# Kernel tuning notes

Measured on AMD Instinct MI355X. Metric: run time of the kernel, lower is better.

Reference implementation:

```python
import jax, jax.numpy as jnp
import numpy as np

N = 100000
E = 600000
H = 128
G = 64          # number of graphs
LN_EPS = 1e-5


def setup_inputs() -> dict:
    key = jax.random.key(0)
    ks = jax.random.split(key, 16)
    node = jax.random.normal(ks[0], (N, H), dtype=jnp.float32)
    edge_index = jax.random.randint(ks[1], (2, E), 0, N, dtype=jnp.int64)
    edge_attr = jax.random.normal(ks[2], (E, 1), dtype=jnp.float32)
    batch_ptr = jnp.sort(jax.random.randint(ks[3], (N,), 0, G, dtype=jnp.int64))
    s = 1.0 / np.sqrt(H)
    params = dict(
        eps=jnp.float32(0.0),  # GINConv train_eps=True, init 0
        W1=jax.random.uniform(ks[4], (H, H), jnp.float32, -s, s),
        b1=jnp.zeros((H,), jnp.float32),
        g1=jnp.ones((H,), jnp.float32), be1=jnp.zeros((H,), jnp.float32),
        W2=jax.random.uniform(ks[5], (H, H), jnp.float32, -s, s),
        b2=jnp.zeros((H,), jnp.float32),
        g2=jnp.ones((H,), jnp.float32), be2=jnp.zeros((H,), jnp.float32),
        W3=jax.random.uniform(ks[6], (H, H), jnp.float32, -s, s),
        b3=jnp.zeros((H,), jnp.float32),
        ln_w=jnp.ones((H,), jnp.float32), ln_b=jnp.zeros((H,), jnp.float32),
    )
    return dict(node=node, edge_index=edge_index, edge_attr=edge_attr,
                batch_ptr=batch_ptr, **params)


def _layernorm(x, g, b):
    mu = x.mean(-1, keepdims=True)
    var = ((x - mu) ** 2).mean(-1, keepdims=True)
    return (x - mu) * jax.lax.rsqrt(var + LN_EPS) * g + b


def _forward(node, edge_index, batch_ptr, eps, W1, b1, g1, be1, W2, b2, g2, be2,
             W3, b3, ln_w, ln_b):
    src, dst = edge_index[0], edge_index[1]
    # GIN sum aggregation: scatter-add neighbor features to targets
    agg = jax.ops.segment_sum(node[src], dst, num_segments=N)  # [N, H]
    h = (1.0 + eps) * node + agg
    # 3-layer MLP (PyG MLP: lin -> LayerNorm -> ReLU, final lin plain)
    h = jax.nn.relu(_layernorm(h @ W1 + b1, g1, be1))
    h = jax.nn.relu(_layernorm(h @ W2 + b2, g2, be2))
    h = h @ W3 + b3
    # PyG graph-mode LayerNorm: normalize over all nodes+features per graph
    cnt = jax.ops.segment_sum(jnp.ones((N,), h.dtype), batch_ptr, num_segments=G)
    norm = jnp.maximum(cnt * H, 1.0)                       # [G]
    mean = jax.ops.segment_sum(h.sum(-1), batch_ptr, num_segments=G) / norm
    hc = h - mean[batch_ptr][:, None]
    var = jax.ops.segment_sum((hc * hc).sum(-1), batch_ptr, num_segments=G) / norm
    out = hc * jax.lax.rsqrt(var + LN_EPS)[batch_ptr][:, None] * ln_w + ln_b
    return jax.nn.relu(out)


def reference(node, edge_index, edge_attr, batch_ptr, eps, W1, b1, g1, be1,
              W2, b2, g2, be2, W3, b3, ln_w, ln_b):
    del edge_attr  # accepted by GIN_Layer.forward but unused
    return _forward(node, edge_index, batch_ptr, eps, W1, b1, g1, be1,
                    W2, b2, g2, be2, W3, b3, ln_w, ln_b)
```

## Files before the change

kernel.cpp:

```cpp
#include <hip/hip_runtime.h>

#define N_NODES 100000
#define N_EDGES 600000
#define H 128
#define G_NUM 64
#define LN_EPS 1e-5f

#define WSTR 136

#define NTILES ((N_NODES + 63) / 64)

#define SCAN_CHUNK 1024
#define SCAN_NB ((N_NODES + SCAN_CHUNK - 1) / SCAN_CHUNK)
#define FILL_NB ((N_EDGES + 255) / 256)
#define WT_NB ((3 * 16384 + 255) / 256)
#define CONV_NB ((N_NODES * 64 + 255) / 256)

typedef __attribute__((ext_vector_type(8))) short short8;
typedef __attribute__((ext_vector_type(4))) float floatx4;

__device__ __forceinline__ unsigned short f2bf(float x) {
    unsigned int u = __float_as_uint(x);
    u += 0x7fffu + ((u >> 16) & 1u);
    return (unsigned short)(u >> 16);
}

__global__ __launch_bounds__(256) void hist_kernel(
    const int* __restrict__ ei, int* __restrict__ deg)
{
    int e = blockIdx.x * 256 + threadIdx.x;
    if (e >= N_EDGES) return;
    atomicAdd(&deg[ei[N_EDGES + e]], 1);
}

__global__ __launch_bounds__(256) void scan1_kernel(
    const int* __restrict__ deg, int* __restrict__ off,
    int* __restrict__ blksum)
{
    __shared__ int sA[256], sB[256];
    const int tid = threadIdx.x;
    const int base = blockIdx.x * SCAN_CHUNK + tid * 4;
    int v[4];
#pragma unroll
    for (int j = 0; j < 4; ++j) {
        int i = base + j;
        v[j] = (i < N_NODES) ? deg[i] : 0;
    }
    int tsum = v[0] + v[1] + v[2] + v[3];
    int* a = sA; int* b = sB;
    a[tid] = tsum;
    __syncthreads();
#pragma unroll
    for (int o = 1; o < 256; o <<= 1) {
        int t = a[tid] + ((tid >= o) ? a[tid - o] : 0);
        b[tid] = t;
        __syncthreads();
        int* tmp = a; a = b; b = tmp;
    }
    int run = a[tid] - tsum;
#pragma unroll
    for (int j = 0; j < 4; ++j) {
        int i = base + j;
        if (i < N_NODES) off[i] = run;
        run += v[j];
    }
    if (tid == 255) blksum[blockIdx.x] = a[255];
}

__global__ __launch_bounds__(256) void scan23_kernel(
    int* __restrict__ off, const int* __restrict__ blksum,
    int* __restrict__ cursor)
{
    __shared__ int sA[128], sB[128];
    const int tid = threadIdx.x;
    if (tid < 128) sA[tid] = (tid < SCAN_NB) ? blksum[tid] : 0;
    __syncthreads();
    int* a = sA; int* b = sB;
#pragma unroll
    for (int o = 1; o < 128; o <<= 1) {
        int t = 0;
        if (tid < 128) t = a[tid] + ((tid >= o) ? a[tid - o] : 0);
        __syncthreads();
        if (tid < 128) b[tid] = t;
        __syncthreads();
        int* tmp = a; a = b; b = tmp;
    }
    int excl = 0;
    if (tid < 128) excl = a[tid] - ((tid < SCAN_NB) ? blksum[tid] : 0);
    __syncthreads();
    if (tid < 128) sA[tid] = excl;
    __syncthreads();

    int i = blockIdx.x * 256 + tid;
    if (i < N_NODES) {
        int val = off[i] + sA[i >> 10];
        off[i] = val;
        cursor[i] = val;
    }
    if (i == 0) off[N_NODES] = N_EDGES;
}

__global__ __launch_bounds__(256) void fill_wt_kernel(
    const int* __restrict__ ei, int* __restrict__ cursor,
    int* __restrict__ csr,
    const float* __restrict__ W1, const float* __restrict__ W2,
    const float* __restrict__ W3, unsigned short* __restrict__ WT,
    const float* __restrict__ node, unsigned int* __restrict__ nodeb)
{
    int gb = blockIdx.x;
    if (gb < FILL_NB) {
        int e = gb * 256 + threadIdx.x;
        if (e >= N_EDGES) return;
        int dst = ei[N_EDGES + e];
        int pos = atomicAdd(&cursor[dst], 1);
        csr[pos] = ei[e];
    } else if (gb < FILL_NB + WT_NB) {
        int idx = (gb - FILL_NB) * 256 + threadIdx.x;
        if (idx >= 3 * 16384) return;
        int l = idx >> 14, r = idx & 16383;
        int frag = r >> 3, j = r & 7;
        int lane = frag & 63, ktnt = frag >> 6;
        int kt = ktnt & 3, nt = ktnt >> 2;
        int c = lane & 15, q = lane >> 4;
        int n = nt * 16 + c;
        int k = kt * 32 + q * 8 + j;
        const float* W = (l == 0) ? W1 : ((l == 1) ? W2 : W3);
        WT[l * 16384 + r] = f2bf(W[k * 128 + n]);
    } else {
        int i = (gb - FILL_NB - WT_NB) * 256 + threadIdx.x;
        if (i >= N_NODES * 64) return;
        float2 v = ((const float2*)node)[i];
        nodeb[i] = (unsigned)f2bf(v.x) | ((unsigned)f2bf(v.y) << 16);
    }
}

__global__ __launch_bounds__(256, 8) void gather_kernel(
    const float* __restrict__ node, const unsigned int* __restrict__ nodeb,
    const int* __restrict__ off, const int* __restrict__ csr,
    const float* __restrict__ epsp, unsigned int* __restrict__ h0)
{
    const int wv = (blockIdx.x * 256 + threadIdx.x) >> 6;
    const int lane = threadIdx.x & 63;
    const int s0 = off[wv], s1 = off[wv + 1];
    const float epsv = 1.0f + epsp[0];
    float2 own = ((const float2*)node)[(size_t)wv * 64 + lane];
    float ax = epsv * own.x, ay = epsv * own.y;
    const int d = s1 - s0;

    for (int base = 0; base < d; base += 64) {
        int m = d - base; if (m > 64) m = 64;
        int idx = 0;
        if (lane < m) idx = csr[s0 + base + lane];
        int j = 0;
        if (nodeb) {
            for (; j + 4 <= m; j += 4) {
                int i0 = __shfl(idx, j),     i1 = __shfl(idx, j + 1);
                int i2 = __shfl(idx, j + 2), i3 = __shfl(idx, j + 3);
                unsigned v0 = nodeb[(size_t)i0 * 64 + lane];
                unsigned v1 = nodeb[(size_t)i1 * 64 + lane];
                unsigned v2 = nodeb[(size_t)i2 * 64 + lane];
                unsigned v3 = nodeb[(size_t)i3 * 64 + lane];
                ax += __uint_as_float(v0 << 16) + __uint_as_float(v1 << 16) +
                      __uint_as_float(v2 << 16) + __uint_as_float(v3 << 16);
                ay += __uint_as_float(v0 & 0xffff0000u) +
                      __uint_as_float(v1 & 0xffff0000u) +
                      __uint_as_float(v2 & 0xffff0000u) +
                      __uint_as_float(v3 & 0xffff0000u);
            }
            for (; j < m; ++j) {
                int i0 = __shfl(idx, j);
                unsigned v0 = nodeb[(size_t)i0 * 64 + lane];
                ax += __uint_as_float(v0 << 16);
                ay += __uint_as_float(v0 & 0xffff0000u);
            }
        } else {
            const float2* np2 = (const float2*)node;
            for (; j + 4 <= m; j += 4) {
                int i0 = __shfl(idx, j),     i1 = __shfl(idx, j + 1);
                int i2 = __shfl(idx, j + 2), i3 = __shfl(idx, j + 3);
                float2 v0 = np2[(size_t)i0 * 64 + lane];
                float2 v1 = np2[(size_t)i1 * 64 + lane];
                float2 v2 = np2[(size_t)i2 * 64 + lane];
                float2 v3 = np2[(size_t)i3 * 64 + lane];
                ax += v0.x + v1.x + v2.x + v3.x;
                ay += v0.y + v1.y + v2.y + v3.y;
            }
            for (; j < m; ++j) {
                int i0 = __shfl(idx, j);
                float2 v0 = np2[(size_t)i0 * 64 + lane];
                ax += v0.x; ay += v0.y;
            }
        }
    }
    h0[(size_t)wv * 64 + lane] = (unsigned)f2bf(ax) | ((unsigned)f2bf(ay) << 16);
}

__device__ __forceinline__ void gemm_frags(const unsigned short* __restrict__ hIn,
                                           const unsigned short* __restrict__ WTl,
                                           floatx4 acc[8], int w, int lane)
{
    const int c = lane & 15, q = lane >> 4;
#pragma unroll
    for (int nt = 0; nt < 8; ++nt) acc[nt] = (floatx4){0.f, 0.f, 0.f, 0.f};
#pragma unroll
    for (int kt = 0; kt < 4; ++kt) {
        short8 a = *(const short8*)&hIn[(w * 16 + c) * WSTR + kt * 32 + q * 8];
#pragma unroll
        for (int nt = 0; nt < 8; ++nt) {
            short8 b = *(const short8*)&WTl[(nt * 256 + kt * 64 + lane) * 8];
            acc[nt] = __builtin_amdgcn_mfma_f32_16x16x32_bf16(a, b, acc[nt], 0, 0, 0);
        }
    }
}

__device__ __forceinline__ void gemm_layer_ln(const unsigned short* __restrict__ hIn,
                                              unsigned short* __restrict__ hOut,
                                              const unsigned short* __restrict__ WTl,
                                              const float* __restrict__ bias,
                                              const float* __restrict__ g,
                                              const float* __restrict__ be,
                                              int w, int lane)
{
    const int c = lane & 15, q = lane >> 4;
    floatx4 acc[8];
    gemm_frags(hIn, WTl, acc, w, lane);

    float sum[4] = {0.f, 0.f, 0.f, 0.f};
    float sq[4]  = {0.f, 0.f, 0.f, 0.f};
#pragma unroll
    for (int nt = 0; nt < 8; ++nt) {
        float bv = bias[nt * 16 + c];
#pragma unroll
        for (int i = 0; i < 4; ++i) {
            float vv = acc[nt][i] + bv;
            acc[nt][i] = vv;
            sum[i] += vv; sq[i] += vv * vv;
        }
    }
#pragma unroll
    for (int m = 1; m < 16; m <<= 1) {
#pragma unroll
        for (int i = 0; i < 4; ++i) {
            sum[i] += __shfl_xor(sum[i], m);
            sq[i]  += __shfl_xor(sq[i], m);
        }
    }
    float mu[4], rstd[4];
#pragma unroll
    for (int i = 0; i < 4; ++i) {
        mu[i]   = sum[i] * (1.0f / 128.0f);
        rstd[i] = rsqrtf(sq[i] * (1.0f / 128.0f) - mu[i] * mu[i] + LN_EPS);
    }
#pragma unroll
    for (int nt = 0; nt < 8; ++nt) {
        float gw = g[nt * 16 + c];
        float bw = be[nt * 16 + c];
#pragma unroll
        for (int i = 0; i < 4; ++i) {
            float val = fmaxf(0.f, (acc[nt][i] - mu[i]) * rstd[i] * gw + bw);
            hOut[(w * 16 + q * 4 + i) * WSTR + nt * 16 + c] = f2bf(val);
        }
    }
}

__global__ __launch_bounds__(256, 4) void mlp_kernel(
    const unsigned int* __restrict__ h0, const unsigned short* __restrict__ WT,
    const float* __restrict__ b1, const float* __restrict__ g1,
    const float* __restrict__ be1,
    const float* __restrict__ b2, const float* __restrict__ g2,
    const float* __restrict__ be2,
    const float* __restrict__ b3, const int* __restrict__ batch,
    float* __restrict__ out, float* __restrict__ gstat)
{
    __shared__ unsigned short hA[64 * WSTR];
    __shared__ unsigned short hB[64 * WSTR];
    __shared__ float prm[7 * 128];
    __shared__ float s_gsum[G_NUM], s_gsq[G_NUM], s_gcnt[G_NUM];

    const int tid = threadIdx.x;
    const int w = tid >> 6, lane = tid & 63;
    const int row0 = blockIdx.x * 64;

    if (tid < G_NUM) { s_gsum[tid] = 0.f; s_gsq[tid] = 0.f; s_gcnt[tid] = 0.f; }
    {
        const float* srcs[7] = {b1, g1, be1, b2, g2, be2, b3};
#pragma unroll
        for (int t = 0; t < 4; ++t) {
            int i = tid + t * 256;
            if (i < 7 * 128) prm[i] = srcs[i >> 7][i & 127];
        }
    }

    {
        const int n0 = row0 + w * 16;
#pragma unroll
        for (int i = 0; i < 16; ++i) {
            int n = n0 + i;
            unsigned int pack = (n < N_NODES) ? h0[(size_t)n * 64 + lane] : 0u;
            ((unsigned int*)&hA[(w * 16 + i) * WSTR])[lane] = pack;
        }
    }
    __syncthreads();

    gemm_layer_ln(hA, hB, WT,         &prm[0],   &prm[128], &prm[256], w, lane);
    gemm_layer_ln(hB, hA, WT + 16384, &prm[384], &prm[512], &prm[640], w, lane);

    {
        const int c = lane & 15, q = lane >> 4;
        floatx4 acc3[8];
        gemm_frags(hA, WT + 32768, acc3, w, lane);
        float sum[4] = {0.f, 0.f, 0.f, 0.f};
        float sq[4]  = {0.f, 0.f, 0.f, 0.f};
#pragma unroll
        for (int nt = 0; nt < 8; ++nt) {
            float bv = prm[768 + nt * 16 + c];
#pragma unroll
            for (int i = 0; i < 4; ++i) {
                float vv = acc3[nt][i] + bv;
                size_t nrow = (size_t)row0 + w * 16 + q * 4 + i;
                if (nrow < N_NODES)
                    out[nrow * H + nt * 16 + c] = vv;
                sum[i] += vv; sq[i] += vv * vv;
            }
        }
#pragma unroll
        for (int m = 1; m < 16; m <<= 1) {
#pragma unroll
            for (int i = 0; i < 4; ++i) {
                sum[i] += __shfl_xor(sum[i], m);
                sq[i]  += __shfl_xor(sq[i], m);
            }
        }
        if (c == 0) {
#pragma unroll
            for (int i = 0; i < 4; ++i) {
                size_t nrow = (size_t)row0 + w * 16 + q * 4 + i;
                if (nrow < N_NODES) {
                    int g = batch[nrow];
                    atomicAdd(&s_gsum[g], sum[i]);
                    atomicAdd(&s_gsq[g], sq[i]);
                    atomicAdd(&s_gcnt[g], 1.0f);
                }
            }
        }
    }
    __syncthreads();
    if (tid < G_NUM && s_gcnt[tid] > 0.f) {
        unsafeAtomicAdd(&gstat[tid], s_gsum[tid]);
        unsafeAtomicAdd(&gstat[G_NUM + tid], s_gsq[tid]);
        unsafeAtomicAdd(&gstat[2 * G_NUM + tid], s_gcnt[tid]);
    }
}

__global__ __launch_bounds__(256) void final_ln_kernel(
    float* __restrict__ h3, const int* __restrict__ batch,
    const float* __restrict__ lnw, const float* __restrict__ lnb,
    const float* __restrict__ gstat)
{
    int idx4 = blockIdx.x * 256 + threadIdx.x;
    if (idx4 >= N_NODES * 32) return;
    int node = idx4 >> 5;
    int c4 = (idx4 & 31) * 4;
    int g = batch[node];
    float s   = gstat[g];
    float qq  = gstat[G_NUM + g];
    float cnt = gstat[2 * G_NUM + g];
    float norm = fmaxf(cnt * (float)H, 1.0f);
    float mean = s / norm;
    float var  = qq / norm - mean * mean;
    float inv  = rsqrtf(var + LN_EPS);
    float4 v = ((const float4*)h3)[idx4];
    float4 w = *(const float4*)&lnw[c4];
    float4 b = *(const float4*)&lnb[c4];
    v.x = fmaxf(0.f, (v.x - mean) * inv * w.x + b.x);
    v.y = fmaxf(0.f, (v.y - mean) * inv * w.y + b.y);
    v.z = fmaxf(0.f, (v.z - mean) * inv * w.z + b.z);
    v.w = fmaxf(0.f, (v.w - mean) * inv * w.w + b.w);
    ((float4*)h3)[idx4] = v;
}

extern "C" void kernel_launch(void* const* d_in, const int* in_sizes, int n_in,
                              void* d_out, int out_size, void* d_ws, size_t ws_size,
                              hipStream_t stream)
{
    const float* node  = (const float*)d_in[0];
    const int*   ei    = (const int*)d_in[1];
    const int*   batch = (const int*)d_in[3];
    const float* epsp  = (const float*)d_in[4];
    const float* W1    = (const float*)d_in[5];
    const float* b1    = (const float*)d_in[6];
    const float* g1    = (const float*)d_in[7];
    const float* be1   = (const float*)d_in[8];
    const float* W2    = (const float*)d_in[9];
    const float* b2    = (const float*)d_in[10];
    const float* g2    = (const float*)d_in[11];
    const float* be2   = (const float*)d_in[12];
    const float* W3    = (const float*)d_in[13];
    const float* b3    = (const float*)d_in[14];
    const float* lnw   = (const float*)d_in[15];
    const float* lnb   = (const float*)d_in[16];

    float* out = (float*)d_out;

    int* base = (int*)d_ws;
    float* gstat  = (float*)d_ws;
    int*   deg    = base + 512;
    int*   off    = deg + N_NODES;
    int*   cursor = off + N_NODES + 1;
    int*   csr    = cursor + N_NODES;
    int*   blksum = csr + N_EDGES;
    unsigned short* WT = (unsigned short*)(base + 900612);
    const size_t nb_off = 900612 + (3 * 16384) / 2;
    unsigned int* nodeb = nullptr;
    unsigned int* h0;
    if (ws_size >= (nb_off + 2ull * N_NODES * 64) * 4) {
        nodeb = (unsigned int*)(base + nb_off);
        h0    = (unsigned int*)(base + nb_off + (size_t)N_NODES * 64);
    } else {
        h0 = (unsigned int*)(base + nb_off);
    }

    hipMemsetAsync(d_ws, 0, (512 + N_NODES) * sizeof(int), stream);

    hist_kernel<<<(N_EDGES + 255) / 256, 256, 0, stream>>>(ei, deg);
    scan1_kernel<<<SCAN_NB, 256, 0, stream>>>(deg, off, blksum);
    scan23_kernel<<<(N_NODES + 255) / 256, 256, 0, stream>>>(off, blksum, cursor);

    int fill_grid = FILL_NB + WT_NB + (nodeb ? CONV_NB : 0);
    fill_wt_kernel<<<fill_grid, 256, 0, stream>>>(ei, cursor, csr,
                                                  W1, W2, W3, WT, node, nodeb);

    gather_kernel<<<(N_NODES * 64) / 256, 256, 0, stream>>>(
        node, nodeb, off, csr, epsp, h0);

    mlp_kernel<<<NTILES, 256, 0, stream>>>(
        h0, WT, b1, g1, be1, b2, g2, be2, b3, batch, out, gstat);

    final_ln_kernel<<<(N_NODES * 32 + 255) / 256, 256, 0, stream>>>(
        out, batch, lnw, lnb, gstat);
}
```

Baseline: 296.1 us.

## Replace CSR build with per-tile edge buckets and fuse gather into MLP

Drops the histogram, two scan kernels and the CSR fill. In their place, edges are bucketed by 64-node destination tile with packed src/local-dst words, and a global overflow list catches buckets past capacity. The separate gather kernel is folded into the MLP kernel: each block accumulates neighbour features into shared memory with LDS float atomics, then converts to bf16 and runs the GEMMs. This removes several launches and the h0 round-trip through global memory, at the cost of shared-memory atomic contention and a slow overflow scan if tiles exceed capacity.

```diff
diff --git a/kernel.cpp b/kernel.cpp
--- a/kernel.cpp
+++ b/kernel.cpp
@@ -9,10 +9,9 @@
 #define WSTR 136
 
 #define NTILES ((N_NODES + 63) / 64)
-
-#define SCAN_CHUNK 1024
-#define SCAN_NB ((N_NODES + SCAN_CHUNK - 1) / SCAN_CHUNK)
-#define FILL_NB ((N_EDGES + 255) / 256)
+#define BKT_CAP 1024
+
+#define BKT_NB ((N_EDGES + 255) / 256)
 #define WT_NB ((3 * 16384 + 255) / 256)
 #define CONV_NB ((N_NODES * 64 + 255) / 256)
 
@@ -25,97 +24,31 @@
     return (unsigned short)(u >> 16);
 }
 
-__global__ __launch_bounds__(256) void hist_kernel(
-    const int* __restrict__ ei, int* __restrict__ deg)
-{
-    int e = blockIdx.x * 256 + threadIdx.x;
-    if (e >= N_EDGES) return;
-    atomicAdd(&deg[ei[N_EDGES + e]], 1);
-}
-
-__global__ __launch_bounds__(256) void scan1_kernel(
-    const int* __restrict__ deg, int* __restrict__ off,
-    int* __restrict__ blksum)
-{
-    __shared__ int sA[256], sB[256];
-    const int tid = threadIdx.x;
-    const int base = blockIdx.x * SCAN_CHUNK + tid * 4;
-    int v[4];
-#pragma unroll
-    for (int j = 0; j < 4; ++j) {
-        int i = base + j;
-        v[j] = (i < N_NODES) ? deg[i] : 0;
-    }
-    int tsum = v[0] + v[1] + v[2] + v[3];
-    int* a = sA; int* b = sB;
-    a[tid] = tsum;
-    __syncthreads();
-#pragma unroll
-    for (int o = 1; o < 256; o <<= 1) {
-        int t = a[tid] + ((tid >= o) ? a[tid - o] : 0);
-        b[tid] = t;
-        __syncthreads();
-        int* tmp = a; a = b; b = tmp;
-    }
-    int run = a[tid] - tsum;
-#pragma unroll
-    for (int j = 0; j < 4; ++j) {
-        int i = base + j;
-        if (i < N_NODES) off[i] = run;
-        run += v[j];
-    }
-    if (tid == 255) blksum[blockIdx.x] = a[255];
-}
-
-__global__ __launch_bounds__(256) void scan23_kernel(
-    int* __restrict__ off, const int* __restrict__ blksum,
-    int* __restrict__ cursor)
-{
-    __shared__ int sA[128], sB[128];
-    const int tid = threadIdx.x;
-    if (tid < 128) sA[tid] = (tid < SCAN_NB) ? blksum[tid] : 0;
-    __syncthreads();
-    int* a = sA; int* b = sB;
-#pragma unroll
-    for (int o = 1; o < 128; o <<= 1) {
-        int t = 0;
-        if (tid < 128) t = a[tid] + ((tid >= o) ? a[tid - o] : 0);
-        __syncthreads();
-        if (tid < 128) b[tid] = t;
-        __syncthreads();
-        int* tmp = a; a = b; b = tmp;
-    }
-    int excl = 0;
-    if (tid < 128) excl = a[tid] - ((tid < SCAN_NB) ? blksum[tid] : 0);
-    __syncthreads();
-    if (tid < 128) sA[tid] = excl;
-    __syncthreads();
-
-    int i = blockIdx.x * 256 + tid;
-    if (i < N_NODES) {
-        int val = off[i] + sA[i >> 10];
-        off[i] = val;
-        cursor[i] = val;
-    }
-    if (i == 0) off[N_NODES] = N_EDGES;
-}
-
-__global__ __launch_bounds__(256) void fill_wt_kernel(
-    const int* __restrict__ ei, int* __restrict__ cursor,
-    int* __restrict__ csr,
+__global__ __launch_bounds__(256) void prep_kernel(
+    const int* __restrict__ ei, int* __restrict__ cnt,
+    unsigned int* __restrict__ bucket, int* __restrict__ ovf_cnt,
+    unsigned int* __restrict__ ovf_pack, int* __restrict__ ovf_tile,
     const float* __restrict__ W1, const float* __restrict__ W2,
     const float* __restrict__ W3, unsigned short* __restrict__ WT,
     const float* __restrict__ node, unsigned int* __restrict__ nodeb)
 {
     int gb = blockIdx.x;
-    if (gb < FILL_NB) {
+    if (gb < BKT_NB) {
         int e = gb * 256 + threadIdx.x;
         if (e >= N_EDGES) return;
-        int dst = ei[N_EDGES + e];
-        int pos = atomicAdd(&cursor[dst], 1);
-        csr[pos] = ei[e];
-    } else if (gb < FILL_NB + WT_NB) {
-        int idx = (gb - FILL_NB) * 256 + threadIdx.x;
+        int src = ei[e], dst = ei[N_EDGES + e];
+        unsigned pack = ((unsigned)src << 6) | (unsigned)(dst & 63);
+        int t = dst >> 6;
+        int pos = atomicAdd(&cnt[t], 1);
+        if (pos < BKT_CAP) {
+            bucket[(size_t)t * BKT_CAP + pos] = pack;
+        } else {
+            int op = atomicAdd(ovf_cnt, 1);
+            ovf_pack[op] = pack;
+            ovf_tile[op] = t;
+        }
+    } else if (gb < BKT_NB + WT_NB) {
+        int idx = (gb - BKT_NB) * 256 + threadIdx.x;
         if (idx >= 3 * 16384) return;
         int l = idx >> 14, r = idx & 16383;
         int frag = r >> 3, j = r & 7;
@@ -127,72 +60,11 @@
         const float* W = (l == 0) ? W1 : ((l == 1) ? W2 : W3);
         WT[l * 16384 + r] = f2bf(W[k * 128 + n]);
     } else {
-        int i = (gb - FILL_NB - WT_NB) * 256 + threadIdx.x;
+        int i = (gb - BKT_NB - WT_NB) * 256 + threadIdx.x;
         if (i >= N_NODES * 64) return;
         float2 v = ((const float2*)node)[i];
         nodeb[i] = (unsigned)f2bf(v.x) | ((unsigned)f2bf(v.y) << 16);
     }
-}
-
-__global__ __launch_bounds__(256, 8) void gather_kernel(
-    const float* __restrict__ node, const unsigned int* __restrict__ nodeb,
-    const int* __restrict__ off, const int* __restrict__ csr,
-    const float* __restrict__ epsp, unsigned int* __restrict__ h0)
-{
-    const int wv = (blockIdx.x * 256 + threadIdx.x) >> 6;
-    const int lane = threadIdx.x & 63;
-    const int s0 = off[wv], s1 = off[wv + 1];
-    const float epsv = 1.0f + epsp[0];
-    float2 own = ((const float2*)node)[(size_t)wv * 64 + lane];
-    float ax = epsv * own.x, ay = epsv * own.y;
-    const int d = s1 - s0;
-
-    for (int base = 0; base < d; base += 64) {
-        int m = d - base; if (m > 64) m = 64;
-        int idx = 0;
-        if (lane < m) idx = csr[s0 + base + lane];
-        int j = 0;
-        if (nodeb) {
-            for (; j + 4 <= m; j += 4) {
-                int i0 = __shfl(idx, j),     i1 = __shfl(idx, j + 1);
-                int i2 = __shfl(idx, j + 2), i3 = __shfl(idx, j + 3);
-                unsigned v0 = nodeb[(size_t)i0 * 64 + lane];
-                unsigned v1 = nodeb[(size_t)i1 * 64 + lane];
-                unsigned v2 = nodeb[(size_t)i2 * 64 + lane];
-                unsigned v3 = nodeb[(size_t)i3 * 64 + lane];
-                ax += __uint_as_float(v0 << 16) + __uint_as_float(v1 << 16) +
-                      __uint_as_float(v2 << 16) + __uint_as_float(v3 << 16);
-                ay += __uint_as_float(v0 & 0xffff0000u) +
-                      __uint_as_float(v1 & 0xffff0000u) +
-                      __uint_as_float(v2 & 0xffff0000u) +
-                      __uint_as_float(v3 & 0xffff0000u);
-            }
-            for (; j < m; ++j) {
-                int i0 = __shfl(idx, j);
-                unsigned v0 = nodeb[(size_t)i0 * 64 + lane];
-                ax += __uint_as_float(v0 << 16);
-                ay += __uint_as_float(v0 & 0xffff0000u);
-            }
-        } else {
-            const float2* np2 = (const float2*)node;
-            for (; j + 4 <= m; j += 4) {
-                int i0 = __shfl(idx, j),     i1 = __shfl(idx, j + 1);
-                int i2 = __shfl(idx, j + 2), i3 = __shfl(idx, j + 3);
-                float2 v0 = np2[(size_t)i0 * 64 + lane];
-                float2 v1 = np2[(size_t)i1 * 64 + lane];
-                float2 v2 = np2[(size_t)i2 * 64 + lane];
-                float2 v3 = np2[(size_t)i3 * 64 + lane];
-                ax += v0.x + v1.x + v2.x + v3.x;
-                ay += v0.y + v1.y + v2.y + v3.y;
-            }
-            for (; j < m; ++j) {
-                int i0 = __shfl(idx, j);
-                float2 v0 = np2[(size_t)i0 * 64 + lane];
-                ax += v0.x; ay += v0.y;
-            }
-        }
-    }
-    h0[(size_t)wv * 64 + lane] = (unsigned)f2bf(ax) | ((unsigned)f2bf(ay) << 16);
 }
 
 __device__ __forceinline__ void gemm_frags(const unsigned short* __restrict__ hIn,
@@ -263,8 +135,12 @@
     }
 }
 
-__global__ __launch_bounds__(256, 4) void mlp_kernel(
-    const unsigned int* __restrict__ h0, const unsigned short* __restrict__ WT,
+__global__ __launch_bounds__(256, 4) void fused_kernel(
+    const float* __restrict__ node, const unsigned int* __restrict__ nodeb,
+    const int* __restrict__ cnt, const unsigned int* __restrict__ bucket,
+    const int* __restrict__ ovf_cnt, const unsigned int* __restrict__ ovf_pack,
+    const int* __restrict__ ovf_tile, const float* __restrict__ epsp,
+    const unsigned short* __restrict__ WT,
     const float* __restrict__ b1, const float* __restrict__ g1,
     const float* __restrict__ be1,
     const float* __restrict__ b2, const float* __restrict__ g2,
@@ -272,35 +148,117 @@
     const float* __restrict__ b3, const int* __restrict__ batch,
     float* __restrict__ out, float* __restrict__ gstat)
 {
-    __shared__ unsigned short hA[64 * WSTR];
-    __shared__ unsigned short hB[64 * WSTR];
+    __shared__ float U[8704];
     __shared__ float prm[7 * 128];
     __shared__ float s_gsum[G_NUM], s_gsq[G_NUM], s_gcnt[G_NUM];
 
     const int tid = threadIdx.x;
     const int w = tid >> 6, lane = tid & 63;
-    const int row0 = blockIdx.x * 64;
-
+    const int t = blockIdx.x;
+    const int row0 = t * 64;
+
+#pragma unroll
+    for (int i = 0; i < 34; ++i) U[tid + i * 256] = 0.f;
     if (tid < G_NUM) { s_gsum[tid] = 0.f; s_gsq[tid] = 0.f; s_gcnt[tid] = 0.f; }
     {
         const float* srcs[7] = {b1, g1, be1, b2, g2, be2, b3};
 #pragma unroll
-        for (int t = 0; t < 4; ++t) {
-            int i = tid + t * 256;
+        for (int k = 0; k < 4; ++k) {
+            int i = tid + k * 256;
             if (i < 7 * 128) prm[i] = srcs[i >> 7][i & 127];
         }
     }
+    __syncthreads();
+
+    float* accE = U;
+    float* accO = U + 4096;
+    const float2* np2 = (const float2*)node;
 
     {
-        const int n0 = row0 + w * 16;
-#pragma unroll
-        for (int i = 0; i < 16; ++i) {
-            int n = n0 + i;
-            unsigned int pack = (n < N_NODES) ? h0[(size_t)n * 64 + lane] : 0u;
-            ((unsigned int*)&hA[(w * 16 + i) * WSTR])[lane] = pack;
+        int m = cnt[t]; if (m > BKT_CAP) m = BKT_CAP;
+        const unsigned* bkt = bucket + (size_t)t * BKT_CAP;
+        for (int b0 = w * 64; b0 < m; b0 += 256) {
+            int mm = m - b0; if (mm > 64) mm = 64;
+            unsigned pk = (lane < mm) ? bkt[b0 + lane] : 0u;
+            int j = 0;
+            if (nodeb) {
+                for (; j + 4 <= mm; j += 4) {
+                    unsigned p0 = __shfl(pk, j),     p1 = __shfl(pk, j + 1);
+                    unsigned p2 = __shfl(pk, j + 2), p3 = __shfl(pk, j + 3);
+                    unsigned v0 = nodeb[(size_t)(p0 >> 6) * 64 + lane];
+                    unsigned v1 = nodeb[(size_t)(p1 >> 6) * 64 + lane];
+                    unsigned v2 = nodeb[(size_t)(p2 >> 6) * 64 + lane];
+                    unsigned v3 = nodeb[(size_t)(p3 >> 6) * 64 + lane];
+                    atomicAdd(&accE[(p0 & 63) * 64 + lane], __uint_as_float(v0 << 16));
+                    atomicAdd(&accO[(p0 & 63) * 64 + lane], __uint_as_float(v0 & 0xffff0000u));
+                    atomicAdd(&accE[(p1 & 63) * 64 + lane], __uint_as_float(v1 << 16));
+                    atomicAdd(&accO[(p1 & 63) * 64 + lane], __uint_as_float(v1 & 0xffff0000u));
+                    atomicAdd(&accE[(p2 & 63) * 64 + lane], __uint_as_float(v2 << 16));
+                    atomicAdd(&accO[(p2 & 63) * 64 + lane], __uint_as_float(v2 & 0xffff0000u));
+                    atomicAdd(&accE[(p3 & 63) * 64 + lane], __uint_as_float(v3 << 16));
+                    atomicAdd(&accO[(p3 & 63) * 64 + lane], __uint_as_float(v3 & 0xffff0000u));
+                }
+                for (; j < mm; ++j) {
+                    unsigned p0 = __shfl(pk, j);
+                    unsigned v0 = nodeb[(size_t)(p0 >> 6) * 64 + lane];
+                    atomicAdd(&accE[(p0 & 63) * 64 + lane], __uint_as_float(v0 << 16));
+                    atomicAdd(&accO[(p0 & 63) * 64 + lane], __uint_as_float(v0 & 0xffff0000u));
+                }
+            } else {
+                for (; j < mm; ++j) {
+                    unsigned p0 = __shfl(pk, j);
+                    float2 v = np2[(size_t)(p0 >> 6) * 64 + lane];
+                    atomicAdd(&accE[(p0 & 63) * 64 + lane], v.x);
+                    atomicAdd(&accO[(p0 & 63) * 64 + lane], v.y);
+                }
+            }
+        }
+        int oc = *ovf_cnt;
+        for (int b0 = w * 64; b0 < oc; b0 += 256) {
+            int mm = oc - b0; if (mm > 64) mm = 64;
+            int tt = -1; unsigned pk = 0u;
+            if (lane < mm) { tt = ovf_tile[b0 + lane]; pk = ovf_pack[b0 + lane]; }
+            for (int j = 0; j < mm; ++j) {
+                if (__shfl(tt, j) != t) continue;
+                unsigned p0 = __shfl(pk, j);
+                float vx, vy;
+                if (nodeb) {
+                    unsigned v = nodeb[(size_t)(p0 >> 6) * 64 + lane];
+                    vx = __uint_as_float(v << 16);
+                    vy = __uint_as_float(v & 0xffff0000u);
+                } else {
+                    float2 v = np2[(size_t)(p0 >> 6) * 64 + lane];
+                    vx = v.x; vy = v.y;
+                }
+                atomicAdd(&accE[(p0 & 63) * 64 + lane], vx);
+                atomicAdd(&accO[(p0 & 63) * 64 + lane], vy);
+            }
         }
     }
     __syncthreads();
+
+    const float epsv = 1.0f + epsp[0];
+    float rx[16], ry[16];
+#pragma unroll
+    for (int i = 0; i < 16; ++i) {
+        int r = w * 16 + i;
+        int n = row0 + r;
+        float ax = accE[r * 64 + lane], ay = accO[r * 64 + lane];
+        if (n < N_NODES) {
+            float2 o = np2[(size_t)n * 64 + lane];
+            ax += epsv * o.x; ay += epsv * o.y;
+        } else { ax = 0.f; ay = 0.f; }
+        rx[i] = ax; ry[i] = ay;
+    }
+    __syncthreads();
+
+    unsigned short* hA = (unsigned short*)U;
+    unsigned short* hB = (unsigned short*)U + 64 * WSTR;
+#pragma unroll
+    for (int i = 0; i < 16; ++i) {
+        unsigned pack = (unsigned)f2bf(rx[i]) | ((unsigned)f2bf(ry[i]) << 16);
+        ((unsigned int*)&hA[(w * 16 + i) * WSTR])[lane] = pack;
+    }
 
     gemm_layer_ln(hA, hB, WT,         &prm[0],   &prm[128], &prm[256], w, lane);
     gemm_layer_ln(hB, hA, WT + 16384, &prm[384], &prm[512], &prm[640], w, lane);
@@ -403,38 +361,29 @@
     float* out = (float*)d_out;
 
     int* base = (int*)d_ws;
-    float* gstat  = (float*)d_ws;
-    int*   deg    = base + 512;
-    int*   off    = deg + N_NODES;
-    int*   cursor = off + N_NODES + 1;
-    int*   csr    = cursor + N_NODES;
-    int*   blksum = csr + N_EDGES;
-    unsigned short* WT = (unsigned short*)(base + 900612);
-    const size_t nb_off = 900612 + (3 * 16384) / 2;
+    float* gstat   = (float*)d_ws;
+    int*   ovf_cnt = base + 320;
+    int*   cnt     = base + 512;
+    unsigned int* bucket   = (unsigned int*)(base + 2080);
+    unsigned int* ovf_pack = (unsigned int*)(base + 1602592);
+    int*          ovf_tile = base + 2202592;
+    unsigned short* WT     = (unsigned short*)(base + 2802592);
     unsigned int* nodeb = nullptr;
-    unsigned int* h0;
-    if (ws_size >= (nb_off + 2ull * N_NODES * 64) * 4) {
-        nodeb = (unsigned int*)(base + nb_off);
-        h0    = (unsigned int*)(base + nb_off + (size_t)N_NODES * 64);
-    } else {
-        h0 = (unsigned int*)(base + nb_off);
-    }
-
-    hipMemsetAsync(d_ws, 0, (512 + N_NODES) * sizeof(int), stream);
-
-    hist_kernel<<<(N_EDGES + 255) / 256, 256, 0, stream>>>(ei, deg);
-    scan1_kernel<<<SCAN_NB, 256, 0, stream>>>(deg, off, blksum);
-    scan23_kernel<<<(N_NODES + 255) / 256, 256, 0, stream>>>(off, blksum, cursor);
-
-    int fill_grid = FILL_NB + WT_NB + (nodeb ? CONV_NB : 0);
-    fill_wt_kernel<<<fill_grid, 256, 0, stream>>>(ei, cursor, csr,
-                                                  W1, W2, W3, WT, node, nodeb);
-
-    gather_kernel<<<(N_NODES * 64) / 256, 256, 0, stream>>>(
-        node, nodeb, off, csr, epsp, h0);
-
-    mlp_kernel<<<NTILES, 256, 0, stream>>>(
-        h0, WT, b1, g1, be1, b2, g2, be2, b3, batch, out, gstat);
+    {
+        size_t need = (2827168ull + (size_t)N_NODES * 64) * 4;
+        if (ws_size >= need) nodeb = (unsigned int*)(base + 2827168);
+    }
+
+    hipMemsetAsync(d_ws, 0, 2080 * sizeof(int), stream);
+
+    int prep_grid = BKT_NB + WT_NB + (nodeb ? CONV_NB : 0);
+    prep_kernel<<<prep_grid, 256, 0, stream>>>(
+        ei, cnt, bucket, ovf_cnt, ovf_pack, ovf_tile,
+        W1, W2, W3, WT, node, nodeb);
+
+    fused_kernel<<<NTILES, 256, 0, stream>>>(
+        node, nodeb, cnt, bucket, ovf_cnt, ovf_pack, ovf_tile, epsp, WT,
+        b1, g1, be1, b2, g2, be2, b3, batch, out, gstat);
 
     final_ln_kernel<<<(N_NODES * 32 + 255) / 256, 256, 0, stream>>>(
         out, batch, lnw, lnb, gstat);
```

Result: slower. 714.7 us (+141.4%).
